# Kernel optimization log

Measured on AMD Instinct MI355X. Metric: run time of the kernel, lower is better.

The kernel has to match this reference:

```python
import jax, jax.numpy as jnp
import numpy as np

EMBED_DIM = 512
NUM_HEADS = 8
HEAD_DIM = EMBED_DIM // NUM_HEADS
SCALE = HEAD_DIM ** -0.5


def setup_inputs() -> dict:
    key = jax.random.key(0)
    k_x, k_qkv, k_o, k_ob = jax.random.split(key, 4)
    x = jax.random.normal(k_x, (2, 2048, EMBED_DIM), dtype=jnp.float32)
    # torch Linear weight is [out, in]; we store transposed [in, out] for x @ W
    w_qkv = jax.random.normal(k_qkv, (EMBED_DIM, 3 * EMBED_DIM), dtype=jnp.float32) * (EMBED_DIM ** -0.5)
    w_o = jax.random.normal(k_o, (EMBED_DIM, EMBED_DIM), dtype=jnp.float32) * (EMBED_DIM ** -0.5)
    b_o = jax.random.normal(k_ob, (EMBED_DIM,), dtype=jnp.float32) * 0.01
    return {"x": x, "w_qkv": w_qkv, "w_o": w_o, "b_o": b_o}


def reference(x, w_qkv, w_o, b_o):
    b, s, e = x.shape
    qkv = x @ w_qkv  # [b, s, 3e]
    q, k, v = jnp.split(qkv, 3, axis=-1)
    # [b, s, e] -> [b, h, s, d]
    def heads(t):
        return t.reshape(b, s, NUM_HEADS, HEAD_DIM).transpose(0, 2, 1, 3)
    q, k, v = heads(q), heads(k), heads(v)
    scores = jnp.einsum("bhqd,bhkd->bhqk", q, k) * SCALE
    attn = jax.nn.softmax(scores, axis=-1)  # dropout = identity in eval
    out = jnp.einsum("bhqk,bhkd->bhqd", attn, v)
    out = out.transpose(0, 2, 1, 3).reshape(b, s, e)
    return out @ w_o + b_o
```

## Files before the change

### kernel.cpp

```cpp
#include <hip/hip_runtime.h>
#include <stdint.h>


typedef __bf16 bf16x8 __attribute__((ext_vector_type(8)));
typedef __bf16 bf16x4 __attribute__((ext_vector_type(4)));
typedef float f32x4 __attribute__((ext_vector_type(4)));

#define MFMA16(a, b, c) __builtin_amdgcn_mfma_f32_16x16x32_bf16((a), (b), (c), 0, 0, 0)
#define QSC 0.18033688011112042f

__device__ __forceinline__ unsigned short f2bf(float f) {
  union { float f; unsigned int u; } v;
  v.f = f;
  unsigned int u = v.u;
  u += 0x7fffu + ((u >> 16) & 1u);
  return (unsigned short)(u >> 16);
}

__device__ __forceinline__ float fast_exp2(float x) {
#if __has_builtin(__builtin_amdgcn_exp2f)
  return __builtin_amdgcn_exp2f(x);
#else
  return exp2f(x);
#endif
}

__device__ __forceinline__ void gld16(const void* g, void* lds) {
  __builtin_amdgcn_global_load_lds(
      (const __attribute__((address_space(1))) unsigned int*)g,
      (__attribute__((address_space(3))) unsigned int*)lds, 16, 0, 0);
}

__global__ void cvt_kernel(const float* __restrict__ in, unsigned short* __restrict__ out, int n4) {
  int i = blockIdx.x * blockDim.x + threadIdx.x;
  if (i < n4) {
    float4 v = ((const float4*)in)[i];
    ushort4 o;
    o.x = f2bf(v.x); o.y = f2bf(v.y); o.z = f2bf(v.z); o.w = f2bf(v.w);
    ((ushort4*)out)[i] = o;
  }
}

__global__ void tcvt_kernel(const float* __restrict__ in, unsigned short* __restrict__ out, int N) {
  __shared__ unsigned short tile[32][33];
  int tx = threadIdx.x & 31, ty = threadIdx.x >> 5;
  int n0 = blockIdx.x * 32, k0 = blockIdx.y * 32;
#pragma unroll
  for (int i = 0; i < 4; ++i)
    tile[ty + i * 8][tx] = f2bf(in[(k0 + ty + i * 8) * N + n0 + tx]);
  __syncthreads();
#pragma unroll
  for (int i = 0; i < 4; ++i)
    out[(n0 + ty + i * 8) * 512 + k0 + tx] = tile[tx][ty + i * 8];
}

__global__ __launch_bounds__(256, 2) void gemm_qkv(
    const unsigned short* __restrict__ A, const unsigned short* __restrict__ Bt,
    unsigned short* __restrict__ qws, unsigned short* __restrict__ kws,
    unsigned short* __restrict__ vtws) {
  __shared__ __align__(16) unsigned short As[2][128 * 64];
  __shared__ __align__(16) unsigned short Bs[2][128 * 64];
  const int tid = threadIdx.x;
  const int wave = tid >> 6, lane = tid & 63;
  const int quad = lane >> 4, l16 = lane & 15;
  const int waveM = (wave & 1) * 64, waveN = (wave >> 1) * 64;
  const int bm = blockIdx.x, bn = blockIdx.y;

  f32x4 acc[4][4] = {};

  const unsigned short* Ab = A + bm * 128 * 512;
  const unsigned short* Bb = Bt + bn * 128 * 512;

  auto stage = [&](int buf, int k0) {
#pragma unroll
    for (int c = 0; c < 4; ++c) {
      int p = wave * 256 + c * 64 + lane;
      int row = p >> 3;
      int ccl = (p & 7) ^ (row & 7);
      gld16(Ab + row * 512 + k0 + ccl * 8, (char*)(As[buf]) + (wave * 256 + c * 64) * 16);
      gld16(Bb + row * 512 + k0 + ccl * 8, (char*)(Bs[buf]) + (wave * 256 + c * 64) * 16);
    }
  };

  stage(0, 0);
  int cur = 0;
  for (int k0 = 0; k0 < 512; k0 += 64) {
    __syncthreads();
    if (k0 + 64 < 512) stage(cur ^ 1, k0 + 64);
    const unsigned short* Asc = As[cur];
    const unsigned short* Bsc = Bs[cur];
#pragma unroll
    for (int ks = 0; ks < 2; ++ks) {
      bf16x8 af[4], bfr[4];
#pragma unroll
      for (int mb = 0; mb < 4; ++mb) {
        int m = waveM + mb * 16 + l16;
        int cc = (ks * 4 + quad) ^ (m & 7);
        af[mb] = *(const bf16x8*)(Asc + m * 64 + cc * 8);
      }
#pragma unroll
      for (int nb = 0; nb < 4; ++nb) {
        int n = waveN + nb * 16 + l16;
        int cc = (ks * 4 + quad) ^ (n & 7);
        bfr[nb] = *(const bf16x8*)(Bsc + n * 64 + cc * 8);
      }
#pragma unroll
      for (int mb = 0; mb < 4; ++mb)
#pragma unroll
        for (int nb = 0; nb < 4; ++nb)
          acc[mb][nb] = MFMA16(af[mb], bfr[nb], acc[mb][nb]);
    }
    cur ^= 1;
  }

  const int mbase = bm * 128 + waveM;
  const int nbase = bn * 128 + waveN;
  const int region = nbase >> 9;
#pragma unroll
  for (int mb = 0; mb < 4; ++mb) {
    int m0 = mbase + mb * 16 + quad * 4;
    int b = m0 >> 11, s0 = m0 & 2047;
#pragma unroll
    for (int nb = 0; nb < 4; ++nb) {
      int n = nbase + nb * 16 + l16;
      int cix = n & 511;
      int h = cix >> 6, d = cix & 63;
      int bh = b * 8 + h;
      if (region == 0) {
#pragma unroll
        for (int r = 0; r < 4; ++r)
          qws[(bh * 2048 + s0 + r) * 64 + d] = f2bf(acc[mb][nb][r] * QSC);
      } else if (region == 1) {
#pragma unroll
        for (int r = 0; r < 4; ++r)
          kws[(bh * 2048 + s0 + r) * 64 + d] = f2bf(acc[mb][nb][r]);
      } else {
        ushort4 pk;
        pk.x = f2bf(acc[mb][nb][0]);
        pk.y = f2bf(acc[mb][nb][1]);
        pk.z = f2bf(acc[mb][nb][2]);
        pk.w = f2bf(acc[mb][nb][3]);
        *(ushort4*)(vtws + (bh * 64 + d) * 2048 + s0) = pk;
      }
    }
  }
}

__global__ __launch_bounds__(256, 2) void attn_kernel(
    const unsigned short* __restrict__ qws, const unsigned short* __restrict__ kws,
    const unsigned short* __restrict__ vtws, __bf16* __restrict__ opart,
    float* __restrict__ lpart) {
  __shared__ __align__(16) unsigned short Ks[2][64 * 64];
  __shared__ __align__(16) unsigned short Vs[2][64 * 64];
  __shared__ __align__(16) __bf16 Pl[4 * 32 * 72];
  const int tid = threadIdx.x;
  const int wave = tid >> 6, lane = tid & 63;
  const int quad = lane >> 4, l16 = lane & 15;
  const int qb = blockIdx.x, bh = blockIdx.y, split = blockIdx.z;

  const unsigned short* Qb = qws + bh * 2048 * 64;
  const unsigned short* Kb = kws + bh * 2048 * 64;
  const unsigned short* Vb = vtws + bh * 64 * 2048;

  const int qbase = qb * 128 + wave * 32;
  bf16x8 qf[2][2];
#pragma unroll
  for (int s = 0; s < 2; ++s)
#pragma unroll
    for (int h = 0; h < 2; ++h)
      qf[s][h] = *(const bf16x8*)(Qb + (qbase + s * 16 + l16) * 64 + h * 32 + quad * 8);

  float l_lane[2] = {0.f, 0.f};
  f32x4 oacc[2][4] = {};
  __bf16* Pw = Pl + wave * 32 * 72;

  const int kt0 = split * 16;

  auto stage = [&](int buf, int kt) {
#pragma unroll
    for (int c = 0; c < 2; ++c) {
      int p = wave * 128 + c * 64 + lane;
      int row = p >> 3;
      int ccl = (p & 7) ^ (row & 7);
      gld16(Kb + (kt * 64 + row) * 64 + ccl * 8, (char*)(Ks[buf]) + (wave * 128 + c * 64) * 16);
      gld16(Vb + row * 2048 + kt * 64 + ccl * 8, (char*)(Vs[buf]) + (wave * 128 + c * 64) * 16);
    }
  };

  stage(0, kt0);
  int cur = 0;
  for (int i = 0; i < 16; ++i) {
    __syncthreads();
    if (i + 1 < 16) stage(cur ^ 1, kt0 + i + 1);
    const unsigned short* Kst = Ks[cur];
    const unsigned short* Vst = Vs[cur];

#pragma unroll
    for (int nb = 0; nb < 4; ++nb) {
      const int krow = nb * 16 + l16;
      bf16x8 kf0 = *(const bf16x8*)(Kst + krow * 64 + (quad ^ (krow & 7)) * 8);
      bf16x8 kf1 = *(const bf16x8*)(Kst + krow * 64 + ((4 + quad) ^ (krow & 7)) * 8);
#pragma unroll
      for (int s = 0; s < 2; ++s) {
        f32x4 sa = {0.f, 0.f, 0.f, 0.f};
        sa = MFMA16(kf0, qf[s][0], sa);
        sa = MFMA16(kf1, qf[s][1], sa);
        float p0 = fast_exp2(sa[0]), p1 = fast_exp2(sa[1]);
        float p2 = fast_exp2(sa[2]), p3 = fast_exp2(sa[3]);
        l_lane[s] += (p0 + p1) + (p2 + p3);
        bf16x4 pk;
        pk[0] = (__bf16)p0; pk[1] = (__bf16)p1; pk[2] = (__bf16)p2; pk[3] = (__bf16)p3;
        *(bf16x4*)(Pw + (s * 16 + l16) * 72 + nb * 16 + quad * 4) = pk;
      }
    }

#pragma unroll
    for (int ks2 = 0; ks2 < 2; ++ks2) {
      bf16x8 pf0 = *(const bf16x8*)(Pw + l16 * 72 + ks2 * 32 + quad * 8);
      bf16x8 pf1 = *(const bf16x8*)(Pw + (16 + l16) * 72 + ks2 * 32 + quad * 8);
#pragma unroll
      for (int db = 0; db < 4; ++db) {
        const int vrow = db * 16 + l16;
        bf16x8 vf = *(const bf16x8*)(Vst + vrow * 64 + (((ks2 * 4 + quad) ^ (vrow & 7))) * 8);
        oacc[0][db] = MFMA16(pf0, vf, oacc[0][db]);
        oacc[1][db] = MFMA16(pf1, vf, oacc[1][db]);
      }
    }
    cur ^= 1;
  }

  const long ob = (long)(split * 16 + bh) * 2048;
#pragma unroll
  for (int s = 0; s < 2; ++s) {
#pragma unroll
    for (int db = 0; db < 4; ++db)
#pragma unroll
      for (int r = 0; r < 4; ++r) {
        int q = qbase + s * 16 + quad * 4 + r;
        opart[(ob + q) * 64 + db * 16 + l16] = (__bf16)oacc[s][db][r];
      }
    float lf = l_lane[s];
    lf += __shfl_xor(lf, 16);
    lf += __shfl_xor(lf, 32);
    if (quad == 0) lpart[ob + qbase + s * 16 + l16] = lf;
  }
}

__global__ void combine_kernel(const __bf16* __restrict__ opart, const float* __restrict__ lpart,
                               unsigned short* __restrict__ ows) {
  int idx = blockIdx.x * 256 + threadIdx.x;
  int dg = idx & 15;
  int q = (idx >> 4) & 2047;
  int bh = idx >> 15;
  bf16x4 o0 = *(const bf16x4*)(opart + ((long)bh * 2048 + q) * 64 + dg * 4);
  bf16x4 o1 = *(const bf16x4*)(opart + ((long)(16 + bh) * 2048 + q) * 64 + dg * 4);
  float inv = 1.0f / (lpart[bh * 2048 + q] + lpart[16 * 2048 + bh * 2048 + q]);
  bf16x4 o;
#pragma unroll
  for (int i = 0; i < 4; ++i) o[i] = (__bf16)(((float)o0[i] + (float)o1[i]) * inv);
  int b = bh >> 3, h = bh & 7;
  *(bf16x4*)((__bf16*)ows + ((long)(b * 2048 + q)) * 512 + h * 64 + dg * 4) = o;
}

__global__ __launch_bounds__(256, 2) void gemm_out(
    const unsigned short* __restrict__ A, const unsigned short* __restrict__ Bt,
    const float* __restrict__ bias, float* __restrict__ out) {
  __shared__ __align__(16) unsigned short As[2][128 * 64];
  __shared__ __align__(16) unsigned short Bs[2][128 * 64];
  const int tid = threadIdx.x;
  const int wave = tid >> 6, lane = tid & 63;
  const int quad = lane >> 4, l16 = lane & 15;
  const int waveM = (wave & 1) * 64, waveN = (wave >> 1) * 64;
  const int bm = blockIdx.x, bn = blockIdx.y;

  f32x4 acc[4][4] = {};

  const unsigned short* Ab = A + bm * 128 * 512;
  const unsigned short* Bb = Bt + bn * 128 * 512;

  auto stage = [&](int buf, int k0) {
#pragma unroll
    for (int c = 0; c < 4; ++c) {
      int p = wave * 256 + c * 64 + lane;
      int row = p >> 3;
      int ccl = (p & 7) ^ (row & 7);
      gld16(Ab + row * 512 + k0 + ccl * 8, (char*)(As[buf]) + (wave * 256 + c * 64) * 16);
      gld16(Bb + row * 512 + k0 + ccl * 8, (char*)(Bs[buf]) + (wave * 256 + c * 64) * 16);
    }
  };

  stage(0, 0);
  int cur = 0;
  for (int k0 = 0; k0 < 512; k0 += 64) {
    __syncthreads();
    if (k0 + 64 < 512) stage(cur ^ 1, k0 + 64);
    const unsigned short* Asc = As[cur];
    const unsigned short* Bsc = Bs[cur];
#pragma unroll
    for (int ks = 0; ks < 2; ++ks) {
      bf16x8 af[4], bfr[4];
#pragma unroll
      for (int mb = 0; mb < 4; ++mb) {
        int m = waveM + mb * 16 + l16;
        int cc = (ks * 4 + quad) ^ (m & 7);
        af[mb] = *(const bf16x8*)(Asc + m * 64 + cc * 8);
      }
#pragma unroll
      for (int nb = 0; nb < 4; ++nb) {
        int n = waveN + nb * 16 + l16;
        int cc = (ks * 4 + quad) ^ (n & 7);
        bfr[nb] = *(const bf16x8*)(Bsc + n * 64 + cc * 8);
      }
#pragma unroll
      for (int mb = 0; mb < 4; ++mb)
#pragma unroll
        for (int nb = 0; nb < 4; ++nb)
          acc[mb][nb] = MFMA16(af[mb], bfr[nb], acc[mb][nb]);
    }
    cur ^= 1;
  }

  const int mbase = bm * 128 + waveM;
  const int nbase = bn * 128 + waveN;
#pragma unroll
  for (int mb = 0; mb < 4; ++mb) {
#pragma unroll
    for (int nb = 0; nb < 4; ++nb) {
      int n = nbase + nb * 16 + l16;
      float bv = bias[n];
#pragma unroll
      for (int r = 0; r < 4; ++r) {
        int m = mbase + mb * 16 + quad * 4 + r;
        out[m * 512 + n] = acc[mb][nb][r] + bv;
      }
    }
  }
}

extern "C" void kernel_launch(void* const* d_in, const int* in_sizes, int n_in,
                              void* d_out, int out_size, void* d_ws, size_t ws_size,
                              hipStream_t stream) {
  const float* x = (const float*)d_in[0];
  const float* w_qkv = (const float*)d_in[1];
  const float* w_o = (const float*)d_in[2];
  const float* b_o = (const float*)d_in[3];
  float* out = (float*)d_out;

  char* ws = (char*)d_ws;
  unsigned short* woT   = (unsigned short*)(ws + 0);
  unsigned short* qws   = (unsigned short*)(ws + 524288);
  unsigned short* kws   = (unsigned short*)(ws + 4718592);
  unsigned short* vtws  = (unsigned short*)(ws + 8912896);
  unsigned short* ows   = (unsigned short*)(ws + 13107200);
  __bf16*         opart = (__bf16*)(ws + 17301504);
  unsigned short* xb    = (unsigned short*)(ws + 17301504);
  unsigned short* wqkvT = (unsigned short*)(ws + 21495808);
  float*          lpart = (float*)(ws + 25690112);

  cvt_kernel<<<2048, 256, 0, stream>>>(x, xb, 524288);
  tcvt_kernel<<<dim3(48, 16), 256, 0, stream>>>(w_qkv, wqkvT, 1536);
  tcvt_kernel<<<dim3(16, 16), 256, 0, stream>>>(w_o, woT, 512);
  gemm_qkv<<<dim3(32, 12), 256, 0, stream>>>(xb, wqkvT, qws, kws, vtws);
  attn_kernel<<<dim3(16, 16, 2), 256, 0, stream>>>(qws, kws, vtws, opart, lpart);
  combine_kernel<<<2048, 256, 0, stream>>>(opart, lpart, ows);
  gemm_out<<<dim3(32, 4), 256, 0, stream>>>(ows, woT, b_o, out);
}
```

Baseline: 127.0 us.

## Use 32x32 MFMA in attention and keep P in registers via permlane swap

Rewrites the attention inner loop to use 32x32x16 bf16 MFMAs instead of 16x16x32, computing S transposed so the exp'd probabilities can be packed with v_cvt_pk_bf16 and rearranged with v_permlane32_swap. This lets P feed the PV MFMA directly as an operand, dropping the per-wave LDS round trip for P and its shared memory. It also adds s_setprio around the MFMA sections to favour matrix issue. The fragment layout and output indexing are reworked to match, so any mismatch in the lane mapping would give wrong results.

```diff
diff --git a/kernel.cpp b/kernel.cpp
--- a/kernel.cpp
+++ b/kernel.cpp
@@ -5,8 +5,10 @@
 typedef __bf16 bf16x8 __attribute__((ext_vector_type(8)));
 typedef __bf16 bf16x4 __attribute__((ext_vector_type(4)));
 typedef float f32x4 __attribute__((ext_vector_type(4)));
+typedef float f32x16 __attribute__((ext_vector_type(16)));
 
 #define MFMA16(a, b, c) __builtin_amdgcn_mfma_f32_16x16x32_bf16((a), (b), (c), 0, 0, 0)
+#define MFMA32(a, b, c) __builtin_amdgcn_mfma_f32_32x32x16_bf16((a), (b), (c), 0, 0, 0)
 #define QSC 0.18033688011112042f
 
 __device__ __forceinline__ unsigned short f2bf(float f) {
@@ -23,6 +25,12 @@
 #else
   return exp2f(x);
 #endif
+}
+
+__device__ __forceinline__ unsigned cvtpk_bf16(float lo, float hi) {
+  unsigned r;
+  asm("v_cvt_pk_bf16_f32 %0, %1, %2" : "=v"(r) : "v"(lo), "v"(hi));
+  return r;
 }
 
 __device__ __forceinline__ void gld16(const void* g, void* lds) {
@@ -152,10 +160,9 @@
     float* __restrict__ lpart) {
   __shared__ __align__(16) unsigned short Ks[2][64 * 64];
   __shared__ __align__(16) unsigned short Vs[2][64 * 64];
-  __shared__ __align__(16) __bf16 Pl[4 * 32 * 72];
   const int tid = threadIdx.x;
   const int wave = tid >> 6, lane = tid & 63;
-  const int quad = lane >> 4, l16 = lane & 15;
+  const int l31 = lane & 31, hi = lane >> 5, l7 = lane & 7;
   const int qb = blockIdx.x, bh = blockIdx.y, split = blockIdx.z;
 
   const unsigned short* Qb = qws + bh * 2048 * 64;
@@ -163,16 +170,14 @@
   const unsigned short* Vb = vtws + bh * 64 * 2048;
 
   const int qbase = qb * 128 + wave * 32;
-  bf16x8 qf[2][2];
-#pragma unroll
-  for (int s = 0; s < 2; ++s)
-#pragma unroll
-    for (int h = 0; h < 2; ++h)
-      qf[s][h] = *(const bf16x8*)(Qb + (qbase + s * 16 + l16) * 64 + h * 32 + quad * 8);
-
-  float l_lane[2] = {0.f, 0.f};
-  f32x4 oacc[2][4] = {};
-  __bf16* Pw = Pl + wave * 32 * 72;
+
+  bf16x8 qf[4];
+#pragma unroll
+  for (int kc = 0; kc < 4; ++kc)
+    qf[kc] = *(const bf16x8*)(Qb + (qbase + l31) * 64 + kc * 16 + hi * 8);
+
+  float l_lane = 0.f;
+  f32x16 oacc[2] = {};
 
   const int kt0 = split * 16;
 
@@ -195,55 +200,61 @@
     const unsigned short* Kst = Ks[cur];
     const unsigned short* Vst = Vs[cur];
 
-#pragma unroll
-    for (int nb = 0; nb < 4; ++nb) {
-      const int krow = nb * 16 + l16;
-      bf16x8 kf0 = *(const bf16x8*)(Kst + krow * 64 + (quad ^ (krow & 7)) * 8);
-      bf16x8 kf1 = *(const bf16x8*)(Kst + krow * 64 + ((4 + quad) ^ (krow & 7)) * 8);
-#pragma unroll
-      for (int s = 0; s < 2; ++s) {
-        f32x4 sa = {0.f, 0.f, 0.f, 0.f};
-        sa = MFMA16(kf0, qf[s][0], sa);
-        sa = MFMA16(kf1, qf[s][1], sa);
-        float p0 = fast_exp2(sa[0]), p1 = fast_exp2(sa[1]);
-        float p2 = fast_exp2(sa[2]), p3 = fast_exp2(sa[3]);
-        l_lane[s] += (p0 + p1) + (p2 + p3);
-        bf16x4 pk;
-        pk[0] = (__bf16)p0; pk[1] = (__bf16)p1; pk[2] = (__bf16)p2; pk[3] = (__bf16)p3;
-        *(bf16x4*)(Pw + (s * 16 + l16) * 72 + nb * 16 + quad * 4) = pk;
-      }
-    }
-
-#pragma unroll
-    for (int ks2 = 0; ks2 < 2; ++ks2) {
-      bf16x8 pf0 = *(const bf16x8*)(Pw + l16 * 72 + ks2 * 32 + quad * 8);
-      bf16x8 pf1 = *(const bf16x8*)(Pw + (16 + l16) * 72 + ks2 * 32 + quad * 8);
-#pragma unroll
-      for (int db = 0; db < 4; ++db) {
-        const int vrow = db * 16 + l16;
-        bf16x8 vf = *(const bf16x8*)(Vst + vrow * 64 + (((ks2 * 4 + quad) ^ (vrow & 7))) * 8);
-        oacc[0][db] = MFMA16(pf0, vf, oacc[0][db]);
-        oacc[1][db] = MFMA16(pf1, vf, oacc[1][db]);
-      }
-    }
+    bf16x8 pa[4];
+#pragma unroll
+    for (int t = 0; t < 2; ++t) {
+      f32x16 sacc = {};
+      __builtin_amdgcn_s_setprio(1);
+#pragma unroll
+      for (int kc = 0; kc < 4; ++kc) {
+        bf16x8 kf = *(const bf16x8*)(Kst + (t * 32 + l31) * 64 + (((kc * 2 + hi) ^ l7) * 8));
+        sacc = MFMA32(kf, qf[kc], sacc);
+      }
+      __builtin_amdgcn_s_setprio(0);
+      float p[16];
+#pragma unroll
+      for (int r = 0; r < 16; ++r) p[r] = fast_exp2(sacc[r]);
+      float ls = 0.f;
+#pragma unroll
+      for (int r = 0; r < 16; r += 4) ls += ((p[r] + p[r + 1]) + (p[r + 2] + p[r + 3]));
+      l_lane += ls;
+#pragma unroll
+      for (int kcl = 0; kcl < 2; ++kcl) {
+        unsigned c0 = cvtpk_bf16(p[8 * kcl + 0], p[8 * kcl + 1]);
+        unsigned c1 = cvtpk_bf16(p[8 * kcl + 2], p[8 * kcl + 3]);
+        unsigned c2 = cvtpk_bf16(p[8 * kcl + 4], p[8 * kcl + 5]);
+        unsigned c3 = cvtpk_bf16(p[8 * kcl + 6], p[8 * kcl + 7]);
+        asm("v_permlane32_swap_b32 %0, %1" : "+v"(c0), "+v"(c2));
+        asm("v_permlane32_swap_b32 %0, %1" : "+v"(c1), "+v"(c3));
+        union { unsigned u[4]; bf16x8 v; } pk;
+        pk.u[0] = c0; pk.u[1] = c1; pk.u[2] = c2; pk.u[3] = c3;
+        pa[t * 2 + kcl] = pk.v;
+      }
+    }
+
+    __builtin_amdgcn_s_setprio(1);
+#pragma unroll
+    for (int kc2 = 0; kc2 < 4; ++kc2) {
+#pragma unroll
+      for (int dh = 0; dh < 2; ++dh) {
+        bf16x8 vf = *(const bf16x8*)(Vst + (dh * 32 + l31) * 64 + (((kc2 * 2 + hi) ^ l7) * 8));
+        oacc[dh] = MFMA32(pa[kc2], vf, oacc[dh]);
+      }
+    }
+    __builtin_amdgcn_s_setprio(0);
     cur ^= 1;
   }
 
   const long ob = (long)(split * 16 + bh) * 2048;
 #pragma unroll
-  for (int s = 0; s < 2; ++s) {
-#pragma unroll
-    for (int db = 0; db < 4; ++db)
-#pragma unroll
-      for (int r = 0; r < 4; ++r) {
-        int q = qbase + s * 16 + quad * 4 + r;
-        opart[(ob + q) * 64 + db * 16 + l16] = (__bf16)oacc[s][db][r];
-      }
-    float lf = l_lane[s];
-    lf += __shfl_xor(lf, 16);
-    lf += __shfl_xor(lf, 32);
-    if (quad == 0) lpart[ob + qbase + s * 16 + l16] = lf;
-  }
+  for (int dh = 0; dh < 2; ++dh)
+#pragma unroll
+    for (int r = 0; r < 16; ++r) {
+      int ql = (r & 3) + 8 * (r >> 2) + 4 * hi;
+      opart[(ob + qbase + ql) * 64 + dh * 32 + l31] = (__bf16)oacc[dh][r];
+    }
+  l_lane += __shfl_xor(l_lane, 32);
+  if (hi == 0) lpart[ob + qbase + l31] = l_lane;
 }
 
 __global__ void combine_kernel(const __bf16* __restrict__ opart, const float* __restrict__ lpart,
```

New measurement: 126.6 us. About the same (-0.3%).
